# Kernel optimization log

Hardware: AMD Instinct MI355X
Metric: run time of the kernel (lower is better)

## Reference

```python
import jax, jax.numpy as jnp
import numpy as np

B = 16384
N_HDV = 12
N_CAV = 8
STEP = 344  # one_step_obs_dim
ALPHA = 0.2  # GAT leaky-relu slope
NEG = -9e15

# field offsets inside one 344-dim step: hdv[0:72] cav[72:120] lanes[120:228]
# bottle[228:230] road_end[230:232] target[232:234] self[234:247]
# dist_bott[247:249] dist_end[249:251] exe[251:253] gen[253:254]

def _linear(x, W, b):
    return x @ W + b

def _mlp(x, W1, b1, W2, b2):
    return jax.nn.relu(_linear(jax.nn.relu(_linear(x, W1, b1)), W2, b2))

def _gat_layer(h, adj, W, a):
    # e_ij = leakyrelu(a . [Wh_i ; Wh_j]) computed without NxNx2F materialization
    Wh = h @ W                       # [B,N,F]
    F = W.shape[1]
    s_i = Wh @ a[:F]                 # [B,N]
    s_j = Wh @ a[F:]                 # [B,N]
    e = jax.nn.leaky_relu(s_i[:, :, None] + s_j[:, None, :], ALPHA)
    e = jnp.where(adj > 0, e, NEG)
    att = jax.nn.softmax(e, axis=2)  # dropout is identity in eval mode
    return att @ Wh                  # [B,N,F]

def _gat(x, adj, W1, a1, W2, a2, Wo, ao):
    x = jnp.concatenate([_gat_layer(x, adj, W1, a1), _gat_layer(x, adj, W2, a2)], axis=2)
    x = jax.nn.elu(_gat_layer(x, adj, Wo, ao))
    return x.mean(axis=1)

def _star_adj(n):
    # ones with [1:,1:] zeroed -> ego-star graph (plus self row/col of node 0)
    return jnp.ones((n, n), jnp.float32).at[1:, 1:].set(0.0)

def setup_inputs() -> dict:
    key = jax.random.key(0)
    ks = iter(jax.random.split(key, 40))
    def rn(shape, scale=0.1):
        return jax.random.normal(next(ks), shape, jnp.float32) * scale
    return {
        'obs': rn((B, STEP * 6), 1.0),
        'W_se': rn((15, 64)), 'b_se': jnp.zeros((64,), jnp.float32),
        'W_de': rn((64, 32)), 'b_de': jnp.zeros((32,), jnp.float32),
        'Wh1': rn((32, 64)), 'ah1': rn((128,)),
        'Wh2': rn((32, 64)), 'ah2': rn((128,)),
        'Who': rn((128, 64)), 'aho': rn((128,)),
        'Wc1': rn((6, 16)), 'ac1': rn((32,)),
        'Wc2': rn((6, 16)), 'ac2': rn((32,)),
        'Wco': rn((32, 64)), 'aco': rn((128,)),
        'Wl1': rn((108, 64)), 'bl1': jnp.zeros((64,), jnp.float32),
        'Wl2': rn((64, 64)), 'bl2': jnp.zeros((64,), jnp.float32),
        'Wm1': rn((205, 64)), 'bm1': jnp.zeros((64,), jnp.float32),
        'Wm2': rn((64, 64)), 'bm2': jnp.zeros((64,), jnp.float32),
    }

def reference(obs, W_se, b_se, W_de, b_de, Wh1, ah1, Wh2, ah2, Who, aho,
              Wc1, ac1, Wc2, ac2, Wco, aco, Wl1, bl1, Wl2, bl2, Wm1, bm1, Wm2, bm2):
    chunks = [obs[:, t * STEP:(t + 1) * STEP] for t in range(6)]  # hist5..current
    hist = chunks[1:6]  # hist4, hist3, hist2, hist1, current
    cur = chunks[5]

    ego3 = lambda c: c[:, 234:237]
    hdv3 = lambda c: c[:, 0:72].reshape(-1, N_HDV, 6)[:, :, :3]
    lrelu01 = lambda x: jax.nn.leaky_relu(x, 0.1)

    history_ego = jnp.concatenate([ego3(c)[:, None, :] for c in hist], axis=2)  # [B,1,15]
    history_hdv = jnp.concatenate([hdv3(c) for c in hist], axis=2)              # [B,12,15]

    hist_ego_emb = _linear(lrelu01(_linear(history_ego, W_se, b_se)), W_de, b_de)  # [B,1,32]
    hist_hdv_emb = _linear(lrelu01(_linear(history_hdv, W_se, b_se)), W_de, b_de)  # [B,12,32]

    adj_hdv = _star_adj(N_HDV + 1)
    adj_cav = _star_adj(N_CAV + 1)

    combined_hdv = jnp.concatenate([hist_ego_emb, hist_hdv_emb], axis=1)  # [B,13,32]
    hdv_rel = _gat(combined_hdv, adj_hdv, Wh1, ah1, Wh2, ah2, Who, aho)   # [B,64]

    cav_stats = cur[:, 72:120].reshape(-1, N_CAV, 6)
    ego_action = jnp.concatenate(
        [cur[:, 234:237], cur[:, 253:254], cur[:, 251:253]], axis=1)[:, None, :]  # [B,1,6]
    combined_cav = jnp.concatenate([ego_action, cav_stats], axis=1)        # [B,9,6]
    cav_rel = _gat(combined_cav, adj_cav, Wc1, ac1, Wc2, ac2, Wco, aco)    # [B,64]

    lanes = _mlp(cur[:, 120:228], Wl1, bl1, Wl2, bl2)                      # [B,64]
    road = jnp.concatenate([cur[:, 228:230], cur[:, 247:249], cur[:, 230:232],
                            cur[:, 249:251], cur[:, 232:234]], axis=1)     # [B,10]
    combined = jnp.concatenate(
        [hdv_rel, cav_rel, lanes, road, cur[:, 251:253], cur[:, 253:254]], axis=1)  # [B,205]
    return _mlp(combined, Wm1, bm1, Wm2, bm2)  # [B,64]
```

## Files before the change

### kernel.cpp

```cpp
#include <hip/hip_runtime.h>

#define DEV __device__ __forceinline__

typedef _Float16 h2v __attribute__((ext_vector_type(2)));
typedef _Float16 f16x4v __attribute__((ext_vector_type(4)));
typedef float f32x4v __attribute__((ext_vector_type(4)));

DEV unsigned pk2u(float a, float b) {
    return __builtin_bit_cast(unsigned, __builtin_amdgcn_cvt_pkrtz(a, b));
}
DEV float dot2u(unsigned a, unsigned b, float c) {
#if __has_builtin(__builtin_amdgcn_fdot2)
    return __builtin_amdgcn_fdot2(__builtin_bit_cast(h2v, a),
                                  __builtin_bit_cast(h2v, b), c, false);
#else
    float d;
    asm("v_dot2_f32_f16 %0, %1, %2, %3" : "=v"(d) : "v"(a), "v"(b), "v"(c));
    return d;
#endif
}
DEV f16x4v mk4(unsigned a, unsigned b) {
    union { unsigned u[2]; f16x4v h; } t; t.u[0] = a; t.u[1] = b; return t.h;
}

DEV float lrelu(float x, float a) { return x > 0.f ? x : a * x; }
DEV float elu1(float x) { return x > 0.f ? x : (__expf(x) - 1.f); }

#define OSE 0
#define ODE 512
#define OH1 1536
#define OH2 2560
#define OHO 3584
#define OL1 7680
#define OL2 11136
#define OM1 13184
#define OM2 19840
#define OCO 21888
#define WTOT 22912
#define OHA WTOT
#define OCA (WTOT + 64)
#define WTOT2 (WTOT + 80)
#define F1 WTOT2
#define F2 (F1 + 512)
#define F3 (F2 + 1024)
#define F4 (F3 + 3584)
#define FM1 (F4 + 2048)
#define FM2 (FM1 + 6656)
#define FHO (FM2 + 2048)
#define FCO2 (FHO + 4096)
#define FEND2 (FCO2 + 1024)
#define HSH_WS 49152
#define CV2_WS (HSH_WS + 13 * 16384 * 16)
#define STG_WS (CV2_WS + 16384 * 32)
#define STG_N 168

__global__ __launch_bounds__(256) void prep_weights(
    const float* __restrict__ W_se, const float* __restrict__ W_de,
    const float* __restrict__ Wh1, const float* __restrict__ Wh2,
    const float* __restrict__ Who, const float* __restrict__ Wl1,
    const float* __restrict__ Wl2, const float* __restrict__ Wm1,
    const float* __restrict__ Wm2, const float* __restrict__ Wco,
    const float* __restrict__ ah1, const float* __restrict__ ah2,
    const float* __restrict__ ac1, const float* __restrict__ ac2,
    const float* __restrict__ Wc1, const float* __restrict__ Wc2,
    const float* __restrict__ b_se, const float* __restrict__ bl1,
    const float* __restrict__ bm1,
    unsigned* __restrict__ ws)
{
    int i = blockIdx.x * 256 + threadIdx.x;
    if (i >= FEND2) return;
    if (i >= WTOT2) {
        int i2 = i - WTOT2;
        unsigned val;
        if (i2 < 512) {
            int tile = i2 >> 7, rem = i2 & 127, reg = rem >> 6, lane = rem & 63;
            int m = tile * 16 + (lane & 15);
            int k0 = 4 * (lane >> 4) + reg * 2;
            float v0 = (k0 < 15) ? W_se[k0 * 64 + m] : ((k0 == 15) ? b_se[m] : 0.f);
            float v1 = (k0 + 1 < 15) ? W_se[(k0 + 1) * 64 + m] : ((k0 + 1 == 15) ? b_se[m] : 0.f);
            val = pk2u(v0, v1);
        } else if (i2 < 1536) {
            int j = i2 - 512;
            int tile = j >> 7, rem = j & 127, reg = rem >> 6, lane = rem & 63;
            int mt2 = tile >> 2, kt2 = tile & 3;
            int m = mt2 * 16 + (lane & 15);
            int k0 = kt2 * 16 + 4 * (lane >> 4) + reg * 2;
            val = pk2u(W_de[k0 * 32 + m], W_de[(k0 + 1) * 32 + m]);
        } else if (i2 < 5120) {
            int j = i2 - 1536;
            int tile = j >> 7, rem = j & 127, reg = rem >> 6, lane = rem & 63;
            int mt1 = tile / 7, kt1 = tile % 7;
            int m = mt1 * 16 + (lane & 15);
            int k0 = kt1 * 16 + 4 * (lane >> 4) + reg * 2;
            float v0 = (k0 < 108) ? Wl1[k0 * 64 + m] : ((k0 == 108) ? bl1[m] : 0.f);
            float v1 = (k0 + 1 < 108) ? Wl1[(k0 + 1) * 64 + m] : ((k0 + 1 == 108) ? bl1[m] : 0.f);
            val = pk2u(v0, v1);
        } else if (i2 < 7168) {
            int j = i2 - 5120;
            int tile = j >> 7, rem = j & 127, reg = rem >> 6, lane = rem & 63;
            int mt1 = tile >> 2, kt1 = tile & 3;
            int m = mt1 * 16 + (lane & 15);
            int k0 = kt1 * 16 + 4 * (lane >> 4) + reg * 2;
            val = pk2u(Wl2[k0 * 64 + m], Wl2[(k0 + 1) * 64 + m]);
        } else if (i2 < 13824) {
            int j = i2 - 7168;
            int tile = j >> 7, rem = j & 127, reg = rem >> 6, lane = rem & 63;
            int mt1 = tile / 13, kt1 = tile % 13;
            int m = mt1 * 16 + (lane & 15);
            int k0 = kt1 * 16 + 4 * (lane >> 4) + reg * 2;
            float v0 = (k0 < 205) ? Wm1[k0 * 64 + m] : ((k0 == 205) ? bm1[m] : 0.f);
            float v1 = (k0 + 1 < 205) ? Wm1[(k0 + 1) * 64 + m] : ((k0 + 1 == 205) ? bm1[m] : 0.f);
            val = pk2u(v0, v1);
        } else if (i2 < 15872) {
            int j = i2 - 13824;
            int tile = j >> 7, rem = j & 127, reg = rem >> 6, lane = rem & 63;
            int mt1 = tile >> 2, kt1 = tile & 3;
            int m = mt1 * 16 + (lane & 15);
            int k0 = kt1 * 16 + 4 * (lane >> 4) + reg * 2;
            val = pk2u(Wm2[k0 * 64 + m], Wm2[(k0 + 1) * 64 + m]);
        } else if (i2 < 19968) {
            int j = i2 - 15872;
            int tile = j >> 7, rem = j & 127, reg = rem >> 6, lane = rem & 63;
            int mt1 = tile >> 3, kt1 = tile & 7;
            int m = mt1 * 16 + (lane & 15);
            int k0 = kt1 * 16 + 4 * (lane >> 4) + reg * 2;
            val = pk2u(Who[k0 * 64 + m], Who[(k0 + 1) * 64 + m]);
        } else {
            int j = i2 - 19968;
            int tile = j >> 7, rem = j & 127, reg = rem >> 6, lane = rem & 63;
            int mt1 = tile >> 1, kt1 = tile & 1;
            int m = mt1 * 16 + (lane & 15);
            int k0 = kt1 * 16 + 4 * (lane >> 4) + reg * 2;
            val = pk2u(Wco[k0 * 64 + m], Wco[(k0 + 1) * 64 + m]);
        }
        ws[i] = val;
        return;
    }
    if (i >= WTOT) {
        int j = i - WTOT;
        if (j < 64) {
            int vec = j >> 4, c2 = j & 15;
            const float* W = (vec < 2) ? Wh1 : Wh2;
            const float* a = (vec < 2) ? ah1 : ah2;
            int sel = (vec & 1) ? 0 : 64;
            float v0 = 0.f, v1 = 0.f;
            for (int q = 0; q < 64; ++q) {
                v0 += W[(2 * c2) * 64 + q] * a[sel + q];
                v1 += W[(2 * c2 + 1) * 64 + q] * a[sel + q];
            }
            ws[i] = pk2u(v0, v1);
        } else {
            int jj = j - 64;
            int vec = jj >> 2, p = jj & 3;
            const float* W = (vec < 2) ? Wc1 : Wc2;
            const float* a = (vec < 2) ? ac1 : ac2;
            int sel = (vec & 1) ? 0 : 16;
            int k0 = 2 * p, k1 = 2 * p + 1;
            float v0 = 0.f, v1 = 0.f;
            if (k0 < 6) for (int q = 0; q < 16; ++q) v0 += W[k0 * 16 + q] * a[sel + q];
            if (k1 < 6) for (int q = 0; q < 16; ++q) v1 += W[k1 * 16 + q] * a[sel + q];
            ws[i] = pk2u(v0, v1);
        }
        return;
    }
    const float* W; int K, N, j;
    if (i < ODE)      { W = W_se; K = 15;  N = 64; j = i - OSE; }
    else if (i < OH1) { W = W_de; K = 64;  N = 32; j = i - ODE; }
    else if (i < OH2) { W = Wh1;  K = 32;  N = 64; j = i - OH1; }
    else if (i < OHO) { W = Wh2;  K = 32;  N = 64; j = i - OH2; }
    else if (i < OL1) { W = Who;  K = 128; N = 64; j = i - OHO; }
    else if (i < OL2) { W = Wl1;  K = 108; N = 64; j = i - OL1; }
    else if (i < OM1) { W = Wl2;  K = 64;  N = 64; j = i - OL2; }
    else if (i < OM2) { W = Wm1;  K = 205; N = 64; j = i - OM1; }
    else if (i < OCO) { W = Wm2;  K = 64;  N = 64; j = i - OM2; }
    else              { W = Wco;  K = 32;  N = 64; j = i - OCO; }
    int k2 = j / N, n = j % N;
    float v0 = (2 * k2     < K) ? W[(2 * k2)     * N + n] : 0.f;
    float v1 = (2 * k2 + 1 < K) ? W[(2 * k2 + 1) * N + n] : 0.f;
    ws[i] = pk2u(v0, v1);
}

__global__ __launch_bounds__(256) void gemm_pre(
    const float* __restrict__ obs, const unsigned* __restrict__ WS,
    const float* __restrict__ b_de, const float* __restrict__ bl2,
    unsigned* __restrict__ wsh, unsigned* __restrict__ wsc, int split)
{
    const int l = threadIdx.x & 63;
    const int w = threadIdx.x >> 6;
    const int t = blockIdx.x * 4 + w;
    const int lo16 = l & 15, hi4 = l >> 4;

    if (t < split) {
        int g = t * 16 + lo16;
        int e = g / 13, r = g - e * 13;
        const float* o = obs + (size_t)e * 2064;
        unsigned b1[2];
#pragma unroll
        for (int reg = 0; reg < 2; ++reg) {
            float v[2];
#pragma unroll
            for (int h = 0; h < 2; ++h) {
                int k = 4 * hi4 + reg * 2 + h;
                float x;
                if (k < 15) {
                    int tc = k / 3 + 1, ff = k - (k / 3) * 3;
                    int col = (r == 0) ? (234 + ff) : ((r - 1) * 6 + ff);
                    x = o[tc * 344 + col];
                } else x = (k == 15) ? 1.f : 0.f;
                v[h] = x;
            }
            b1[reg] = pk2u(v[0], v[1]);
        }
        f16x4v B1 = mk4(b1[0], b1[1]);
        f32x4v d1[4];
#pragma unroll
        for (int mt = 0; mt < 4; ++mt) {
            f16x4v A = mk4(WS[F1 + mt * 128 + l], WS[F1 + mt * 128 + 64 + l]);
            f32x4v z = {0.f, 0.f, 0.f, 0.f};
            d1[mt] = __builtin_amdgcn_mfma_f32_16x16x16f16(A, B1, z, 0, 0, 0);
        }
        f16x4v B2[4];
#pragma unroll
        for (int kt = 0; kt < 4; ++kt) {
            B2[kt] = mk4(pk2u(lrelu(d1[kt][0], 0.1f), lrelu(d1[kt][1], 0.1f)),
                         pk2u(lrelu(d1[kt][2], 0.1f), lrelu(d1[kt][3], 0.1f)));
        }
#pragma unroll
        for (int mt2 = 0; mt2 < 2; ++mt2) {
            float4 bb = *(const float4*)(b_de + mt2 * 16 + 4 * hi4);
            f32x4v acc = {bb.x, bb.y, bb.z, bb.w};
#pragma unroll
            for (int kt = 0; kt < 4; ++kt) {
                f16x4v A = mk4(WS[F2 + (mt2 * 4 + kt) * 128 + l],
                               WS[F2 + (mt2 * 4 + kt) * 128 + 64 + l]);
                acc = __builtin_amdgcn_mfma_f32_16x16x16f16(A, B2[kt], acc, 0, 0, 0);
            }
            unsigned* dst = wsh + (size_t)g * 16 + mt2 * 8 + 2 * hi4;
            dst[0] = pk2u(acc[0], acc[1]);
            dst[1] = pk2u(acc[2], acc[3]);
        }
    } else {
        int tt = t - split;
        int e = tt * 16 + lo16;
        const float* o = obs + (size_t)e * 2064 + 1840;
        f32x4v acc1[4];
#pragma unroll
        for (int mt = 0; mt < 4; ++mt) acc1[mt] = (f32x4v){0.f, 0.f, 0.f, 0.f};
#pragma unroll
        for (int kt = 0; kt < 7; ++kt) {
            unsigned bu[2];
#pragma unroll
            for (int reg = 0; reg < 2; ++reg) {
                float v[2];
#pragma unroll
                for (int h = 0; h < 2; ++h) {
                    int k = kt * 16 + 4 * hi4 + reg * 2 + h;
                    v[h] = (k < 108) ? o[k] : ((k == 108) ? 1.f : 0.f);
                }
                bu[reg] = pk2u(v[0], v[1]);
            }
            f16x4v Bf = mk4(bu[0], bu[1]);
#pragma unroll
            for (int mt = 0; mt < 4; ++mt) {
                f16x4v A = mk4(WS[F3 + (mt * 7 + kt) * 128 + l],
                               WS[F3 + (mt * 7 + kt) * 128 + 64 + l]);
                acc1[mt] = __builtin_amdgcn_mfma_f32_16x16x16f16(A, Bf, acc1[mt], 0, 0, 0);
            }
        }
        f16x4v B2[4];
#pragma unroll
        for (int kt = 0; kt < 4; ++kt) {
            B2[kt] = mk4(pk2u(fmaxf(acc1[kt][0], 0.f), fmaxf(acc1[kt][1], 0.f)),
                         pk2u(fmaxf(acc1[kt][2], 0.f), fmaxf(acc1[kt][3], 0.f)));
        }
#pragma unroll
        for (int mt = 0; mt < 4; ++mt) {
            float4 bb = *(const float4*)(bl2 + mt * 16 + 4 * hi4);
            f32x4v acc = {bb.x, bb.y, bb.z, bb.w};
#pragma unroll
            for (int kt = 0; kt < 4; ++kt) {
                f16x4v A = mk4(WS[F4 + (mt * 4 + kt) * 128 + l],
                               WS[F4 + (mt * 4 + kt) * 128 + 64 + l]);
                acc = __builtin_amdgcn_mfma_f32_16x16x16f16(A, B2[kt], acc, 0, 0, 0);
            }
            unsigned* dst = wsc + (size_t)e * 32 + mt * 8 + 2 * hi4;
            dst[0] = pk2u(fmaxf(acc[0], 0.f), fmaxf(acc[1], 0.f));
            dst[1] = pk2u(fmaxf(acc[2], 0.f), fmaxf(acc[3], 0.f));
        }
    }
}

__global__ __launch_bounds__(256) void gemm_final(
    const unsigned* __restrict__ WS, const unsigned* __restrict__ stg,
    const unsigned* __restrict__ wsc,
    const float* __restrict__ aho, const float* __restrict__ aco,
    const float* __restrict__ bm2, float* __restrict__ out)
{
    const int l = threadIdx.x & 63;
    const int w = threadIdx.x >> 6;
    const int t = blockIdx.x * 4 + w;
    const int lo16 = l & 15, hi4 = l >> 4;
    const int e = t * 16 + lo16;
    const unsigned* sv = stg + (size_t)e * STG_N;

    f16x4v Bm[13];

    {
        f32x4v a0[4], a1[4];
#pragma unroll
        for (int mt = 0; mt < 4; ++mt) {
            a0[mt] = (f32x4v){0.f, 0.f, 0.f, 0.f};
            a1[mt] = (f32x4v){0.f, 0.f, 0.f, 0.f};
        }
#pragma unroll
        for (int kt = 0; kt < 8; ++kt) {
            f16x4v B0 = mk4(sv[kt * 8 + 2 * hi4], sv[kt * 8 + 2 * hi4 + 1]);
            f16x4v Br = mk4(sv[64 + kt * 8 + 2 * hi4], sv[64 + kt * 8 + 2 * hi4 + 1]);
#pragma unroll
            for (int mt = 0; mt < 4; ++mt) {
                f16x4v A = mk4(WS[FHO + (mt * 8 + kt) * 128 + l],
                               WS[FHO + (mt * 8 + kt) * 128 + 64 + l]);
                a0[mt] = __builtin_amdgcn_mfma_f32_16x16x16f16(A, B0, a0[mt], 0, 0, 0);
                a1[mt] = __builtin_amdgcn_mfma_f32_16x16x16f16(A, Br, a1[mt], 0, 0, 0);
            }
        }
        float si = 0.f, sj = 0.f, sr = 0.f;
#pragma unroll
        for (int mt = 0; mt < 4; ++mt) {
            float4 AL = *(const float4*)(aho + mt * 16 + 4 * hi4);
            float4 AH = *(const float4*)(aho + 64 + mt * 16 + 4 * hi4);
            si += a0[mt][0] * AL.x + a0[mt][1] * AL.y + a0[mt][2] * AL.z + a0[mt][3] * AL.w;
            sj += a0[mt][0] * AH.x + a0[mt][1] * AH.y + a0[mt][2] * AH.z + a0[mt][3] * AH.w;
            sr += a1[mt][0] * AH.x + a1[mt][1] * AH.y + a1[mt][2] * AH.z + a1[mt][3] * AH.w;
        }
        si += __shfl_xor(si, 16); si += __shfl_xor(si, 32);
        sj += __shfl_xor(sj, 16); sj += __shfl_xor(sj, 32);
        sr += __shfl_xor(sr, 16); sr += __shfl_xor(sr, 32);
        float e0 = lrelu(si + sj, 0.2f);
        float er = lrelu(si + sr, 0.2f);
        float m = fmaxf(e0, er);
        float p0 = __expf(e0 - m);
        float pr = __expf(er - m) * 12.f;
        float inv = 1.f / (p0 + pr);
#pragma unroll
        for (int mt = 0; mt < 4; ++mt) {
            float cv[4];
#pragma unroll
            for (int r = 0; r < 4; ++r) {
                float o0 = (p0 * a0[mt][r] + pr * a1[mt][r]) * inv;
                cv[r] = (elu1(o0) + 12.f * elu1(a0[mt][r])) * (1.f / 13.f);
            }
            Bm[mt] = mk4(pk2u(cv[0], cv[1]), pk2u(cv[2], cv[3]));
        }
    }

    {
        f32x4v c0[4], c1[4];
#pragma unroll
        for (int mt = 0; mt < 4; ++mt) {
            c0[mt] = (f32x4v){0.f, 0.f, 0.f, 0.f};
            c1[mt] = (f32x4v){0.f, 0.f, 0.f, 0.f};
        }
#pragma unroll
        for (int kt = 0; kt < 2; ++kt) {
            f16x4v B0 = mk4(sv[128 + kt * 8 + 2 * hi4], sv[128 + kt * 8 + 2 * hi4 + 1]);
            f16x4v Br = mk4(sv[144 + kt * 8 + 2 * hi4], sv[144 + kt * 8 + 2 * hi4 + 1]);
#pragma unroll
            for (int mt = 0; mt < 4; ++mt) {
                f16x4v A = mk4(WS[FCO2 + (mt * 2 + kt) * 128 + l],
                               WS[FCO2 + (mt * 2 + kt) * 128 + 64 + l]);
                c0[mt] = __builtin_amdgcn_mfma_f32_16x16x16f16(A, B0, c0[mt], 0, 0, 0);
                c1[mt] = __builtin_amdgcn_mfma_f32_16x16x16f16(A, Br, c1[mt], 0, 0, 0);
            }
        }
        float si = 0.f, sj = 0.f, sr = 0.f;
#pragma unroll
        for (int mt = 0; mt < 4; ++mt) {
            float4 AL = *(const float4*)(aco + mt * 16 + 4 * hi4);
            float4 AH = *(const float4*)(aco + 64 + mt * 16 + 4 * hi4);
            si += c0[mt][0] * AL.x + c0[mt][1] * AL.y + c0[mt][2] * AL.z + c0[mt][3] * AL.w;
            sj += c0[mt][0] * AH.x + c0[mt][1] * AH.y + c0[mt][2] * AH.z + c0[mt][3] * AH.w;
            sr += c1[mt][0] * AH.x + c1[mt][1] * AH.y + c1[mt][2] * AH.z + c1[mt][3] * AH.w;
        }
        si += __shfl_xor(si, 16); si += __shfl_xor(si, 32);
        sj += __shfl_xor(sj, 16); sj += __shfl_xor(sj, 32);
        sr += __shfl_xor(sr, 16); sr += __shfl_xor(sr, 32);
        float e0 = lrelu(si + sj, 0.2f);
        float er = lrelu(si + sr, 0.2f);
        float m = fmaxf(e0, er);
        float p0 = __expf(e0 - m);
        float pr = __expf(er - m) * 8.f;
        float inv = 1.f / (p0 + pr);
#pragma unroll
        for (int mt = 0; mt < 4; ++mt) {
            float cv[4];
#pragma unroll
            for (int r = 0; r < 4; ++r) {
                float o0 = (p0 * c0[mt][r] + pr * c1[mt][r]) * inv;
                cv[r] = (elu1(o0) + 8.f * elu1(c0[mt][r])) * (1.f / 9.f);
            }
            Bm[4 + mt] = mk4(pk2u(cv[0], cv[1]), pk2u(cv[2], cv[3]));
        }
    }

#pragma unroll
    for (int kt = 8; kt < 12; ++kt)
        Bm[kt] = mk4(wsc[(size_t)e * 32 + (kt - 8) * 8 + 2 * hi4],
                     wsc[(size_t)e * 32 + (kt - 8) * 8 + 2 * hi4 + 1]);
    Bm[12] = mk4(sv[160 + 2 * hi4], sv[160 + 2 * hi4 + 1]);

    f32x4v acc1[4];
#pragma unroll
    for (int mt = 0; mt < 4; ++mt) acc1[mt] = (f32x4v){0.f, 0.f, 0.f, 0.f};
#pragma unroll
    for (int kt = 0; kt < 13; ++kt) {
#pragma unroll
        for (int mt = 0; mt < 4; ++mt) {
            f16x4v A = mk4(WS[FM1 + (mt * 13 + kt) * 128 + l],
                           WS[FM1 + (mt * 13 + kt) * 128 + 64 + l]);
            acc1[mt] = __builtin_amdgcn_mfma_f32_16x16x16f16(A, Bm[kt], acc1[mt], 0, 0, 0);
        }
    }
    f16x4v B2[4];
#pragma unroll
    for (int kt = 0; kt < 4; ++kt) {
        B2[kt] = mk4(pk2u(fmaxf(acc1[kt][0], 0.f), fmaxf(acc1[kt][1], 0.f)),
                     pk2u(fmaxf(acc1[kt][2], 0.f), fmaxf(acc1[kt][3], 0.f)));
    }
#pragma unroll
    for (int mt = 0; mt < 4; ++mt) {
        float4 bb = *(const float4*)(bm2 + mt * 16 + 4 * hi4);
        f32x4v acc = {bb.x, bb.y, bb.z, bb.w};
#pragma unroll
        for (int kt = 0; kt < 4; ++kt) {
            f16x4v A = mk4(WS[FM2 + (mt * 4 + kt) * 128 + l],
                           WS[FM2 + (mt * 4 + kt) * 128 + 64 + l]);
            acc = __builtin_amdgcn_mfma_f32_16x16x16f16(A, B2[kt], acc, 0, 0, 0);
        }
        float4 st;
        st.x = fmaxf(acc[0], 0.f);
        st.y = fmaxf(acc[1], 0.f);
        st.z = fmaxf(acc[2], 0.f);
        st.w = fmaxf(acc[3], 0.f);
        *(float4*)(out + (size_t)e * 64 + mt * 16 + 4 * hi4) = st;
    }
}

#define HSHF  0
#define CURS  624
#define HCF   864
#define SCR   936
#define S12H  1000
#define QCF   1032
#define HCH   1048
#define HSH2  1216
#define ELEM_U 1480

__global__ __launch_bounds__(256, 4) void pred_kernel(
    const float* __restrict__ obs,
    const unsigned* __restrict__ WS,
    const unsigned* __restrict__ WSH,
    const float* __restrict__ Wc1, const float* __restrict__ Wc2,
    unsigned* __restrict__ STG)
{
    const int l = threadIdx.x & 63;
    const int w = threadIdx.x >> 6;
    const int b = blockIdx.x * 4 + w;
    const float* o = obs + (size_t)b * 2064;
    unsigned* stg = STG + (size_t)b * STG_N;

    __shared__ unsigned lds[4 * ELEM_U];
    unsigned* SU = lds + w * ELEM_U;
    float* SF = (float*)SU;

    for (int i = l; i < 184; i += 64) SF[CURS + i] = o[1792 + i];
    for (int i = l; i < 208; i += 64) {
        int rr = i >> 4, c2 = i & 15;
        unsigned v = WSH[(size_t)(b * 13 + rr) * 16 + c2];
        SU[HSH2 + rr * 20 + c2] = v;
        union { unsigned u; h2v h; } tc; tc.u = v;
        float2 f2; f2.x = (float)tc.h[0]; f2.y = (float)tc.h[1];
        *(float2*)(SF + HSHF + rr * 32 + 2 * c2) = f2;
    }
    for (int i = l; i < 72; i += 64) {
        int r = i >> 3, f = i & 7;
        float v = 0.f;
        if (f < 6) {
            if (r == 0) {
                int idx = (f < 3) ? (162 + f) : ((f == 3) ? 181 : (175 + f));
                v = SF[CURS + idx];
            } else {
                v = SF[CURS + (r - 1) * 6 + f];
            }
        }
        SF[HCF + i] = v;
    }
    if (l < 36) {
        int r = l >> 2, p = l & 3;
        float v0 = SF[HCF + r * 8 + 2 * p];
        float v1 = SF[HCF + r * 8 + 2 * p + 1];
        SU[HCH + r * 4 + p] = pk2u(v0, v1);
    }

    {
        int g = l >> 4, r = l & 15;
        float sc = 0.f;
        if (g < 2) {
            if (r < 14) {
                int ridx = (r == 13) ? 0 : r;
                const uint4* hr = (const uint4*)(SU + HSH2 + ridx * 20);
                const uint4* av = (const uint4*)(WS + OHA + g * 32 + ((r == 13) ? 16 : 0));
                uint4 h0 = hr[0], h1 = hr[1], h2 = hr[2], h3 = hr[3];
                uint4 a0 = av[0], a1 = av[1], a2 = av[2], a3 = av[3];
                float sa = 0.f, sb = 0.f;
                sa = dot2u(h0.x, a0.x, sa); sa = dot2u(h0.y, a0.y, sa);
                sa = dot2u(h0.z, a0.z, sa); sa = dot2u(h0.w, a0.w, sa);
                sb = dot2u(h1.x, a1.x, sb); sb = dot2u(h1.y, a1.y, sb);
                sb = dot2u(h1.z, a1.z, sb); sb = dot2u(h1.w, a1.w, sb);
                sa = dot2u(h2.x, a2.x, sa); sa = dot2u(h2.y, a2.y, sa);
                sa = dot2u(h2.z, a2.z, sa); sa = dot2u(h2.w, a2.w, sa);
                sb = dot2u(h3.x, a3.x, sb); sb = dot2u(h3.y, a3.y, sb);
                sb = dot2u(h3.z, a3.z, sb); sb = dot2u(h3.w, a3.w, sb);
                sc = sa + sb;
            }
        } else {
            if (r < 10) {
                int ridx = (r == 9) ? 0 : r;
                const uint4* hr = (const uint4*)(SU + HCH + ridx * 4);
                const uint4* cv = (const uint4*)(WS + OCA + (g - 2) * 8 + ((r == 9) ? 4 : 0));
                uint4 h = hr[0];
                uint4 a = cv[0];
                sc = dot2u(h.x, a.x, sc);
                sc = dot2u(h.y, a.y, sc);
                sc = dot2u(h.z, a.z, sc);
            }
        }
        SF[SCR + l] = sc;
    }

    if (l < 32) {
        const float4* sq = (const float4*)(SF + SCR);
        float4 a0 = sq[0], a1 = sq[1], a2 = sq[2], a3 = sq[3];
        float4 b0 = sq[4], b1 = sq[5], b2 = sq[6], b3 = sq[7];
        float p1[13] = {a0.x,a0.y,a0.z,a0.w,a1.x,a1.y,a1.z,a1.w,a2.x,a2.y,a2.z,a2.w,a3.x};
        float si1 = a3.y;
        float p2[13] = {b0.x,b0.y,b0.z,b0.w,b1.x,b1.y,b1.z,b1.w,b2.x,b2.y,b2.z,b2.w,b3.x};
        float si2 = b3.y;
        float m1 = -1e30f, m2 = -1e30f;
#pragma unroll
        for (int r = 0; r < 13; ++r) {
            p1[r] = lrelu(si1 + p1[r], 0.2f);
            p2[r] = lrelu(si2 + p2[r], 0.2f);
            m1 = fmaxf(m1, p1[r]);
            m2 = fmaxf(m2, p2[r]);
        }
        float den1 = 0.f, den2 = 0.f;
#pragma unroll
        for (int r = 0; r < 13; ++r) {
            p1[r] = __expf(p1[r] - m1);
            p2[r] = __expf(p2[r] - m2);
            den1 += p1[r];
            den2 += p2[r];
        }
        float rd1 = 1.f / den1, rd2 = 1.f / den2;
        int c = l;
        float s1 = 0.f, s2 = 0.f;
#pragma unroll
        for (int r = 0; r < 13; ++r) {
            float h = SF[HSHF + r * 32 + c];
            s1 = __builtin_fmaf(p1[r], h, s1);
            s2 = __builtin_fmaf(p2[r], h, s2);
        }
        s1 *= rd1; s2 *= rd2;
        float s1n = __shfl_xor(s1, 1), s2n = __shfl_xor(s2, 1);
        if (!(l & 1)) {
            SU[S12H + (c >> 1)] = pk2u(s1, s1n);
            SU[S12H + 16 + (c >> 1)] = pk2u(s2, s2n);
        }
    } else {
        const float4* sq = (const float4*)(SF + SCR + 32);
        float4 a0 = sq[0], a1 = sq[1], a2 = sq[2];
        float4 b0 = sq[4], b1 = sq[5], b2 = sq[6];
        float q1[9] = {a0.x,a0.y,a0.z,a0.w,a1.x,a1.y,a1.z,a1.w,a2.x};
        float sic1 = a2.y;
        float q2[9] = {b0.x,b0.y,b0.z,b0.w,b1.x,b1.y,b1.z,b1.w,b2.x};
        float sic2 = b2.y;
        float m1 = -1e30f, m2 = -1e30f;
#pragma unroll
        for (int r = 0; r < 9; ++r) {
            q1[r] = lrelu(sic1 + q1[r], 0.2f);
            q2[r] = lrelu(sic2 + q2[r], 0.2f);
            m1 = fmaxf(m1, q1[r]);
            m2 = fmaxf(m2, q2[r]);
        }
        float den1 = 0.f, den2 = 0.f;
#pragma unroll
        for (int r = 0; r < 9; ++r) {
            q1[r] = __expf(q1[r] - m1);
            q2[r] = __expf(q2[r] - m2);
            den1 += q1[r];
            den2 += q2[r];
        }
        float rd1 = 1.f / den1, rd2 = 1.f / den2;
        int k = l & 15;
        int gat = (l >> 4) & 1;
        if (k < 6) {
            float su = 0.f;
#pragma unroll
            for (int r = 0; r < 9; ++r) {
                float h = SF[HCF + r * 8 + k];
                su = __builtin_fmaf(gat ? q2[r] : q1[r], h, su);
            }
            su *= gat ? rd2 : rd1;
            SF[QCF + gat * 8 + k] = su;
        }
    }

    {
        float o1 = 0.f, w1 = 0.f, o2 = 0.f, w2 = 0.f;
        const uint4* s1v = (const uint4*)(SU + S12H);
        const uint4* s2v = (const uint4*)(SU + S12H + 16);
        const uint4* h0v = (const uint4*)(SU + HSH2);
#pragma unroll
        for (int kc = 0; kc < 4; ++kc) {
            uint4 sa = s1v[kc], sb = s2v[kc], hz = h0v[kc];
            unsigned wa0 = WS[OH1 + (kc * 4 + 0) * 64 + l], wb0 = WS[OH2 + (kc * 4 + 0) * 64 + l];
            unsigned wa1 = WS[OH1 + (kc * 4 + 1) * 64 + l], wb1 = WS[OH2 + (kc * 4 + 1) * 64 + l];
            unsigned wa2 = WS[OH1 + (kc * 4 + 2) * 64 + l], wb2 = WS[OH2 + (kc * 4 + 2) * 64 + l];
            unsigned wa3 = WS[OH1 + (kc * 4 + 3) * 64 + l], wb3 = WS[OH2 + (kc * 4 + 3) * 64 + l];
            o1 = dot2u(sa.x, wa0, o1); o1 = dot2u(sa.y, wa1, o1);
            o1 = dot2u(sa.z, wa2, o1); o1 = dot2u(sa.w, wa3, o1);
            w1 = dot2u(hz.x, wa0, w1); w1 = dot2u(hz.y, wa1, w1);
            w1 = dot2u(hz.z, wa2, w1); w1 = dot2u(hz.w, wa3, w1);
            o2 = dot2u(sb.x, wb0, o2); o2 = dot2u(sb.y, wb1, o2);
            o2 = dot2u(sb.z, wb2, o2); o2 = dot2u(sb.w, wb3, o2);
            w2 = dot2u(hz.x, wb0, w2); w2 = dot2u(hz.y, wb1, w2);
            w2 = dot2u(hz.z, wb2, w2); w2 = dot2u(hz.w, wb3, w2);
        }
        float o1n = __shfl_xor(o1, 1), o2n = __shfl_xor(o2, 1);
        float w1n = __shfl_xor(w1, 1), w2n = __shfl_xor(w2, 1);
        if (!(l & 1)) {
            stg[(l >> 1)] = pk2u(o1, o1n);
            stg[32 + (l >> 1)] = pk2u(o2, o2n);
            stg[64 + (l >> 1)] = pk2u(w1, w1n);
            stg[96 + (l >> 1)] = pk2u(w2, w2n);
        }
    }

    {
        int g = l >> 4, c = l & 15;
        const float* vec = (g & 1) ? (SF + HCF) : (SF + QCF + (g >> 1) * 8);
        const float* Wc = (g < 2) ? Wc1 : Wc2;
        float acc = 0.f;
#pragma unroll
        for (int k = 0; k < 6; ++k)
            acc = __builtin_fmaf(vec[k], Wc[k * 16 + c], acc);
        float an = __shfl_xor(acc, 1);
        if (!(l & 1))
            stg[128 + ((g & 1) ? 16 : 0) + (g >> 1) * 8 + (c >> 1)] = pk2u(acc, an);
    }

    {
        float v = 0.f;
        if (l < 13) {
            int idx;
            if (l < 10) {
                int p = l >> 1, odd = l & 1;
                idx = ((p & 1) ? 175 : 156) + (p >> 1) * 2 + odd;
            } else {
                idx = 169 + l;
            }
            v = SF[CURS + idx];
        } else if (l == 13) {
            v = 1.0f;
        }
        float vn = __shfl_xor(v, 1);
        if (l < 16 && !(l & 1)) stg[160 + (l >> 1)] = pk2u(v, vn);
    }
}

extern "C" void kernel_launch(void* const* d_in, const int* in_sizes, int n_in,
                              void* d_out, int out_size, void* d_ws, size_t ws_size,
                              hipStream_t stream) {
    const float* obs  = (const float*)d_in[0];
    const float* W_se = (const float*)d_in[1];
    const float* b_se = (const float*)d_in[2];
    const float* W_de = (const float*)d_in[3];
    const float* b_de = (const float*)d_in[4];
    const float* Wh1  = (const float*)d_in[5];
    const float* ah1  = (const float*)d_in[6];
    const float* Wh2  = (const float*)d_in[7];
    const float* ah2  = (const float*)d_in[8];
    const float* Who  = (const float*)d_in[9];
    const float* aho  = (const float*)d_in[10];
    const float* Wc1  = (const float*)d_in[11];
    const float* ac1  = (const float*)d_in[12];
    const float* Wc2  = (const float*)d_in[13];
    const float* ac2  = (const float*)d_in[14];
    const float* Wco  = (const float*)d_in[15];
    const float* aco  = (const float*)d_in[16];
    const float* Wl1  = (const float*)d_in[17];
    const float* bl1  = (const float*)d_in[18];
    const float* Wl2  = (const float*)d_in[19];
    const float* bl2  = (const float*)d_in[20];
    const float* Wm1  = (const float*)d_in[21];
    const float* bm1  = (const float*)d_in[22];
    const float* Wm2  = (const float*)d_in[23];
    const float* bm2  = (const float*)d_in[24];

    unsigned* ws = (unsigned*)d_ws;
    prep_weights<<<(FEND2 + 255) / 256, 256, 0, stream>>>(
        W_se, W_de, Wh1, Wh2, Who, Wl1, Wl2, Wm1, Wm2, Wco,
        ah1, ah2, ac1, ac2, Wc1, Wc2, b_se, bl1, bm1, ws);

    int B = in_sizes[0] / 2064;
    int t1 = (13 * B) / 16;
    int t2 = B / 16;
    gemm_pre<<<(t1 + t2) / 4, 256, 0, stream>>>(
        obs, ws, b_de, bl2, ws + HSH_WS, ws + CV2_WS, t1);

    pred_kernel<<<B / 4, 256, 0, stream>>>(
        obs, ws, ws + HSH_WS, Wc1, Wc2, ws + STG_WS);

    gemm_final<<<(B / 16) / 4, 256, 0, stream>>>(
        ws, ws + STG_WS, ws + CV2_WS, aho, aco, bm2, (float*)d_out);
}
```

Measured before the change: 59.85 us.

## Move GAT head projections from per-element dot2 into batched MFMA in final kernel

The per-element projections of the aggregated first-layer GAT features (s1/s2 and ego-hidden through Wh1/Wh2, and the CAV Wc1/Wc2 projections) move out of pred_kernel, where they ran as scalar dot2 and FMA loops. They are now computed in gemm_final as 16x16x16 MFMAs over 16 batch elements at a time, and the results feed straight into the output-layer MFMAs as packed B operands. The staging buffer shrinks from 168 to 64 words per element, which cuts global traffic between kernels. The trade-off is extra register pressure in gemm_final and an additional read of the ego hidden state from the HSH workspace. One Wh2 packing line contains an odd nullptr check on Wh1 that never fires.

After: 79.57 us. 1.33x slower.

```diff
diff --git a/kernel.cpp b/kernel.cpp
--- a/kernel.cpp
+++ b/kernel.cpp
@@ -21,6 +21,9 @@
 }
 DEV f16x4v mk4(unsigned a, unsigned b) {
     union { unsigned u[2]; f16x4v h; } t; t.u[0] = a; t.u[1] = b; return t.h;
+}
+DEV f16x4v pkD(f32x4v d) {
+    return mk4(pk2u(d[0], d[1]), pk2u(d[2], d[3]));
 }
 
 DEV float lrelu(float x, float a) { return x > 0.f ? x : a * x; }
@@ -48,11 +51,15 @@
 #define FM2 (FM1 + 6656)
 #define FHO (FM2 + 2048)
 #define FCO2 (FHO + 4096)
-#define FEND2 (FCO2 + 1024)
+#define FH1T (FCO2 + 1024)
+#define FH2T (FH1T + 1024)
+#define FC1T (FH2T + 1024)
+#define FC2T (FC1T + 128)
+#define FEND3 (FC2T + 128)
 #define HSH_WS 49152
 #define CV2_WS (HSH_WS + 13 * 16384 * 16)
 #define STG_WS (CV2_WS + 16384 * 32)
-#define STG_N 168
+#define STG_N 64
 
 __global__ __launch_bounds__(256) void prep_weights(
     const float* __restrict__ W_se, const float* __restrict__ W_de,
@@ -68,7 +75,7 @@
     unsigned* __restrict__ ws)
 {
     int i = blockIdx.x * 256 + threadIdx.x;
-    if (i >= FEND2) return;
+    if (i >= FEND3) return;
     if (i >= WTOT2) {
         int i2 = i - WTOT2;
         unsigned val;
@@ -125,13 +132,43 @@
             int m = mt1 * 16 + (lane & 15);
             int k0 = kt1 * 16 + 4 * (lane >> 4) + reg * 2;
             val = pk2u(Who[k0 * 64 + m], Who[(k0 + 1) * 64 + m]);
-        } else {
+        } else if (i2 < 20992) {
             int j = i2 - 19968;
             int tile = j >> 7, rem = j & 127, reg = rem >> 6, lane = rem & 63;
             int mt1 = tile >> 1, kt1 = tile & 1;
             int m = mt1 * 16 + (lane & 15);
             int k0 = kt1 * 16 + 4 * (lane >> 4) + reg * 2;
             val = pk2u(Wco[k0 * 64 + m], Wco[(k0 + 1) * 64 + m]);
+        } else if (i2 < 22016) {
+            int j = i2 - 20992;
+            int tile = j >> 7, rem = j & 127, reg = rem >> 6, lane = rem & 63;
+            int mt1 = tile >> 1, kt1 = tile & 1;
+            int m = mt1 * 16 + (lane & 15);
+            int k0 = kt1 * 16 + 4 * (lane >> 4) + reg * 2;
+            val = pk2u(Wh1[k0 * 64 + m], Wh1[(k0 + 1) * 64 + m]);
+        } else if (i2 < 23040) {
+            int j = i2 - 22016;
+            int tile = j >> 7, rem = j & 127, reg = rem >> 6, lane = rem & 63;
+            int mt1 = tile >> 1, kt1 = tile & 1;
+            int m = mt1 * 16 + (lane & 15);
+            int k0 = kt1 * 16 + 4 * (lane >> 4) + reg * 2;
+            val = pk2u(Wh1 == nullptr ? 0.f : Wh2[k0 * 64 + m], Wh2[(k0 + 1) * 64 + m]);
+        } else if (i2 < 23168) {
+            int j = i2 - 23040;
+            int reg = (j >> 6) & 1, lane = j & 63;
+            int m = lane & 15;
+            int k0 = 4 * (lane >> 4) + reg * 2;
+            float v0 = (k0 < 6) ? Wc1[k0 * 16 + m] : 0.f;
+            float v1 = (k0 + 1 < 6) ? Wc1[(k0 + 1) * 16 + m] : 0.f;
+            val = pk2u(v0, v1);
+        } else {
+            int j = i2 - 23168;
+            int reg = (j >> 6) & 1, lane = j & 63;
+            int m = lane & 15;
+            int k0 = 4 * (lane >> 4) + reg * 2;
+            float v0 = (k0 < 6) ? Wc2[k0 * 16 + m] : 0.f;
+            float v1 = (k0 + 1 < 6) ? Wc2[(k0 + 1) * 16 + m] : 0.f;
+            val = pk2u(v0, v1);
         }
         ws[i] = val;
         return;
@@ -292,7 +329,7 @@
 
 __global__ __launch_bounds__(256) void gemm_final(
     const unsigned* __restrict__ WS, const unsigned* __restrict__ stg,
-    const unsigned* __restrict__ wsc,
+    const unsigned* __restrict__ wsc, const unsigned* __restrict__ wsh,
     const float* __restrict__ aho, const float* __restrict__ aco,
     const float* __restrict__ bm2, float* __restrict__ out)
 {
@@ -305,6 +342,36 @@
 
     f16x4v Bm[13];
 
+    f16x4v Bho0[8], Bhor[8];
+    {
+        f16x4v Bs1[2], Bs2[2], Bh0[2];
+#pragma unroll
+        for (int kt = 0; kt < 2; ++kt) {
+            Bs1[kt] = mk4(sv[kt * 8 + 2 * hi4], sv[kt * 8 + 2 * hi4 + 1]);
+            Bs2[kt] = mk4(sv[16 + kt * 8 + 2 * hi4], sv[16 + kt * 8 + 2 * hi4 + 1]);
+            Bh0[kt] = mk4(wsh[(size_t)e * 208 + kt * 8 + 2 * hi4],
+                          wsh[(size_t)e * 208 + kt * 8 + 2 * hi4 + 1]);
+        }
+#pragma unroll
+        for (int mt = 0; mt < 4; ++mt) {
+            f32x4v o1 = {0.f,0.f,0.f,0.f}, w1 = {0.f,0.f,0.f,0.f};
+            f32x4v o2 = {0.f,0.f,0.f,0.f}, w2 = {0.f,0.f,0.f,0.f};
+#pragma unroll
+            for (int kt = 0; kt < 2; ++kt) {
+                f16x4v A1 = mk4(WS[FH1T + (mt * 2 + kt) * 128 + l],
+                                WS[FH1T + (mt * 2 + kt) * 128 + 64 + l]);
+                f16x4v A2 = mk4(WS[FH2T + (mt * 2 + kt) * 128 + l],
+                                WS[FH2T + (mt * 2 + kt) * 128 + 64 + l]);
+                o1 = __builtin_amdgcn_mfma_f32_16x16x16f16(A1, Bs1[kt], o1, 0, 0, 0);
+                w1 = __builtin_amdgcn_mfma_f32_16x16x16f16(A1, Bh0[kt], w1, 0, 0, 0);
+                o2 = __builtin_amdgcn_mfma_f32_16x16x16f16(A2, Bs2[kt], o2, 0, 0, 0);
+                w2 = __builtin_amdgcn_mfma_f32_16x16x16f16(A2, Bh0[kt], w2, 0, 0, 0);
+            }
+            Bho0[mt] = pkD(o1);   Bho0[4 + mt] = pkD(o2);
+            Bhor[mt] = pkD(w1);   Bhor[4 + mt] = pkD(w2);
+        }
+    }
+
     {
         f32x4v a0[4], a1[4];
 #pragma unroll
@@ -314,14 +381,12 @@
         }
 #pragma unroll
         for (int kt = 0; kt < 8; ++kt) {
-            f16x4v B0 = mk4(sv[kt * 8 + 2 * hi4], sv[kt * 8 + 2 * hi4 + 1]);
-            f16x4v Br = mk4(sv[64 + kt * 8 + 2 * hi4], sv[64 + kt * 8 + 2 * hi4 + 1]);
 #pragma unroll
             for (int mt = 0; mt < 4; ++mt) {
                 f16x4v A = mk4(WS[FHO + (mt * 8 + kt) * 128 + l],
                                WS[FHO + (mt * 8 + kt) * 128 + 64 + l]);
-                a0[mt] = __builtin_amdgcn_mfma_f32_16x16x16f16(A, B0, a0[mt], 0, 0, 0);
-                a1[mt] = __builtin_amdgcn_mfma_f32_16x16x16f16(A, Br, a1[mt], 0, 0, 0);
+                a0[mt] = __builtin_amdgcn_mfma_f32_16x16x16f16(A, Bho0[kt], a0[mt], 0, 0, 0);
+                a1[mt] = __builtin_amdgcn_mfma_f32_16x16x16f16(A, Bhor[kt], a1[mt], 0, 0, 0);
             }
         }
         float si = 0.f, sj = 0.f, sr = 0.f;
@@ -354,6 +419,20 @@
         }
     }
 
+    f16x4v Bco0[2], Bcor[2];
+    {
+        f16x4v Bq1 = mk4(sv[32 + 2 * hi4], sv[32 + 2 * hi4 + 1]);
+        f16x4v Bq2 = mk4(sv[40 + 2 * hi4], sv[40 + 2 * hi4 + 1]);
+        f16x4v Bhc = mk4(sv[48 + 2 * hi4], sv[48 + 2 * hi4 + 1]);
+        f16x4v A1 = mk4(WS[FC1T + l], WS[FC1T + 64 + l]);
+        f16x4v A2 = mk4(WS[FC2T + l], WS[FC2T + 64 + l]);
+        f32x4v z = {0.f, 0.f, 0.f, 0.f};
+        Bco0[0] = pkD(__builtin_amdgcn_mfma_f32_16x16x16f16(A1, Bq1, z, 0, 0, 0));
+        Bco0[1] = pkD(__builtin_amdgcn_mfma_f32_16x16x16f16(A2, Bq2, z, 0, 0, 0));
+        Bcor[0] = pkD(__builtin_amdgcn_mfma_f32_16x16x16f16(A1, Bhc, z, 0, 0, 0));
+        Bcor[1] = pkD(__builtin_amdgcn_mfma_f32_16x16x16f16(A2, Bhc, z, 0, 0, 0));
+    }
+
     {
         f32x4v c0[4], c1[4];
 #pragma unroll
@@ -363,14 +442,12 @@
         }
 #pragma unroll
         for (int kt = 0; kt < 2; ++kt) {
-            f16x4v B0 = mk4(sv[128 + kt * 8 + 2 * hi4], sv[128 + kt * 8 + 2 * hi4 + 1]);
-            f16x4v Br = mk4(sv[144 + kt * 8 + 2 * hi4], sv[144 + kt * 8 + 2 * hi4 + 1]);
 #pragma unroll
             for (int mt = 0; mt < 4; ++mt) {
                 f16x4v A = mk4(WS[FCO2 + (mt * 2 + kt) * 128 + l],
                                WS[FCO2 + (mt * 2 + kt) * 128 + 64 + l]);
-                c0[mt] = __builtin_amdgcn_mfma_f32_16x16x16f16(A, B0, c0[mt], 0, 0, 0);
-                c1[mt] = __builtin_amdgcn_mfma_f32_16x16x16f16(A, Br, c1[mt], 0, 0, 0);
+                c0[mt] = __builtin_amdgcn_mfma_f32_16x16x16f16(A, Bco0[kt], c0[mt], 0, 0, 0);
+                c1[mt] = __builtin_amdgcn_mfma_f32_16x16x16f16(A, Bcor[kt], c1[mt], 0, 0, 0);
             }
         }
         float si = 0.f, sj = 0.f, sr = 0.f;
@@ -407,7 +484,7 @@
     for (int kt = 8; kt < 12; ++kt)
         Bm[kt] = mk4(wsc[(size_t)e * 32 + (kt - 8) * 8 + 2 * hi4],
                      wsc[(size_t)e * 32 + (kt - 8) * 8 + 2 * hi4 + 1]);
-    Bm[12] = mk4(sv[160 + 2 * hi4], sv[160 + 2 * hi4 + 1]);
+    Bm[12] = mk4(sv[56 + 2 * hi4], sv[56 + 2 * hi4 + 1]);
 
     f32x4v acc1[4];
 #pragma unroll
@@ -450,8 +527,6 @@
 #define CURS  624
 #define HCF   864
 #define SCR   936
-#define S12H  1000
-#define QCF   1032
 #define HCH   1048
 #define HSH2  1216
 #define ELEM_U 1480
@@ -460,7 +535,6 @@
     const float* __restrict__ obs,
     const unsigned* __restrict__ WS,
     const unsigned* __restrict__ WSH,
-    const float* __restrict__ Wc1, const float* __restrict__ Wc2,
     unsigned* __restrict__ STG)
 {
     const int l = threadIdx.x & 63;
@@ -500,6 +574,28 @@
         float v0 = SF[HCF + r * 8 + 2 * p];
         float v1 = SF[HCF + r * 8 + 2 * p + 1];
         SU[HCH + r * 4 + p] = pk2u(v0, v1);
+    }
+    {
+        float v = (l < 8) ? SF[HCF + l] : 0.f;
+        float vn = __shfl_xor(v, 1);
+        if (l < 16 && !(l & 1)) stg[48 + (l >> 1)] = pk2u(v, vn);
+    }
+    {
+        float v = 0.f;
+        if (l < 13) {
+            int idx;
+            if (l < 10) {
+                int p = l >> 1, odd = l & 1;
+                idx = ((p & 1) ? 175 : 156) + (p >> 1) * 2 + odd;
+            } else {
+                idx = 169 + l;
+            }
+            v = SF[CURS + idx];
+        } else if (l == 13) {
+            v = 1.0f;
+        }
+        float vn = __shfl_xor(v, 1);
+        if (l < 16 && !(l & 1)) stg[56 + (l >> 1)] = pk2u(v, vn);
     }
 
     {
@@ -574,8 +670,8 @@
         s1 *= rd1; s2 *= rd2;
         float s1n = __shfl_xor(s1, 1), s2n = __shfl_xor(s2, 1);
         if (!(l & 1)) {
-            SU[S12H + (c >> 1)] = pk2u(s1, s1n);
-            SU[S12H + 16 + (c >> 1)] = pk2u(s2, s2n);
+            stg[(c >> 1)] = pk2u(s1, s1n);
+            stg[16 + (c >> 1)] = pk2u(s2, s2n);
         }
     } else {
         const float4* sq = (const float4*)(SF + SCR + 32);
@@ -604,78 +700,17 @@
         float rd1 = 1.f / den1, rd2 = 1.f / den2;
         int k = l & 15;
         int gat = (l >> 4) & 1;
+        float su = 0.f;
         if (k < 6) {
-            float su = 0.f;
 #pragma unroll
             for (int r = 0; r < 9; ++r) {
                 float h = SF[HCF + r * 8 + k];
                 su = __builtin_fmaf(gat ? q2[r] : q1[r], h, su);
             }
             su *= gat ? rd2 : rd1;
-            SF[QCF + gat * 8 + k] = su;
-        }
-    }
-
-    {
-        float o1 = 0.f, w1 = 0.f, o2 = 0.f, w2 = 0.f;
-        const uint4* s1v = (const uint4*)(SU + S12H);
-        const uint4* s2v = (const uint4*)(SU + S12H + 16);
-        const uint4* h0v = (const uint4*)(SU + HSH2);
-#pragma unroll
-        for (int kc = 0; kc < 4; ++kc) {
-            uint4 sa = s1v[kc], sb = s2v[kc], hz = h0v[kc];
-            unsigned wa0 = WS[OH1 + (kc * 4 + 0) * 64 + l], wb0 = WS[OH2 + (kc * 4 + 0) * 64 + l];
-            unsigned wa1 = WS[OH1 + (kc * 4 + 1) * 64 + l], wb1 = WS[OH2 + (kc * 4 + 1) * 64 + l];
-            unsigned wa2 = WS[OH1 + (kc * 4 + 2) * 64 + l], wb2 = WS[OH2 + (kc * 4 + 2) * 64 + l];
-            unsigned wa3 = WS[OH1 + (kc * 4 + 3) * 64 + l], wb3 = WS[OH2 + (kc * 4 + 3) * 64 + l];
-            o1 = dot2u(sa.x, wa0, o1); o1 = dot2u(sa.y, wa1, o1);
-            o1 = dot2u(sa.z, wa2, o1); o1 = dot2u(sa.w, wa3, o1);
-            w1 = dot2u(hz.x, wa0, w1); w1 = dot2u(hz.y, wa1, w1);
-            w1 = dot2u(hz.z, wa2, w1); w1 = dot2u(hz.w, wa3, w1);
-            o2 = dot2u(sb.x, wb0, o2); o2 = dot2u(sb.y, wb1, o2);
-            o2 = dot2u(sb.z, wb2, o2); o2 = dot2u(sb.w, wb3, o2);
-            w2 = dot2u(hz.x, wb0, w2); w2 = dot2u(hz.y, wb1, w2);
-            w2 = dot2u(hz.z, wb2, w2); w2 = dot2u(hz.w, wb3, w2);
-        }
-        float o1n = __shfl_xor(o1, 1), o2n = __shfl_xor(o2, 1);
-        float w1n = __shfl_xor(w1, 1), w2n = __shfl_xor(w2, 1);
-        if (!(l & 1)) {
-            stg[(l >> 1)] = pk2u(o1, o1n);
-            stg[32 + (l >> 1)] = pk2u(o2, o2n);
-            stg[64 + (l >> 1)] = pk2u(w1, w1n);
-            stg[96 + (l >> 1)] = pk2u(w2, w2n);
-        }
-    }
-
-    {
-        int g = l >> 4, c = l & 15;
-        const float* vec = (g & 1) ? (SF + HCF) : (SF + QCF + (g >> 1) * 8);
-        const float* Wc = (g < 2) ? Wc1 : Wc2;
-        float acc = 0.f;
-#pragma unroll
-        for (int k = 0; k < 6; ++k)
-            acc = __builtin_fmaf(vec[k], Wc[k * 16 + c], acc);
-        float an = __shfl_xor(acc, 1);
-        if (!(l & 1))
-            stg[128 + ((g & 1) ? 16 : 0) + (g >> 1) * 8 + (c >> 1)] = pk2u(acc, an);
-    }
-
-    {
-        float v = 0.f;
-        if (l < 13) {
-            int idx;
-            if (l < 10) {
-                int p = l >> 1, odd = l & 1;
-                idx = ((p & 1) ? 175 : 156) + (p >> 1) * 2 + odd;
-            } else {
-                idx = 169 + l;
-            }
-            v = SF[CURS + idx];
-        } else if (l == 13) {
-            v = 1.0f;
-        }
-        float vn = __shfl_xor(v, 1);
-        if (l < 16 && !(l & 1)) stg[160 + (l >> 1)] = pk2u(v, vn);
+        }
+        float sun = __shfl_xor(su, 1);
+        if (!(l & 1)) stg[32 + gat * 8 + (k >> 1)] = pk2u(su, sun);
     }
 }
 
@@ -709,7 +744,7 @@
     const float* bm2  = (const float*)d_in[24];
 
     unsigned* ws = (unsigned*)d_ws;
-    prep_weights<<<(FEND2 + 255) / 256, 256, 0, stream>>>(
+    prep_weights<<<(FEND3 + 255) / 256, 256, 0, stream>>>(
         W_se, W_de, Wh1, Wh2, Who, Wl1, Wl2, Wm1, Wm2, Wco,
         ah1, ah2, ac1, ac2, Wc1, Wc2, b_se, bl1, bm1, ws);
 
@@ -720,8 +755,8 @@
         obs, ws, b_de, bl2, ws + HSH_WS, ws + CV2_WS, t1);
 
     pred_kernel<<<B / 4, 256, 0, stream>>>(
-        obs, ws, ws + HSH_WS, Wc1, Wc2, ws + STG_WS);
+        obs, ws, ws + HSH_WS, ws + STG_WS);
 
     gemm_final<<<(B / 16) / 4, 256, 0, stream>>>(
-        ws, ws + STG_WS, ws + CV2_WS, aho, aco, bm2, (float*)d_out);
-}
+        ws, ws + STG_WS, ws + CV2_WS, ws + HSH_WS, aho, aco, bm2, (float*)d_out);
+}
```
